# Performance work log

Measured on AMD Instinct MI355X. Metric: run time of the kernel, lower is better.

Reference implementation:

```python
import jax, jax.numpy as jnp
import numpy as np

D_MODEL = 1024
NUM_HEADS = 16
D_K = D_MODEL // NUM_HEADS


def setup_inputs() -> dict:
    key = jax.random.key(0)
    k1, k2, k3 = jax.random.split(key, 3)
    x = jax.random.normal(k1, (2, 2048, D_MODEL), dtype=jnp.float32)
    # torch Linear(d, 3d): weight shape [3d, d], y = x @ W.T
    W_QKV = jax.random.normal(k2, (3 * D_MODEL, D_MODEL), dtype=jnp.float32) * (1.0 / np.sqrt(D_MODEL))
    W_O = jax.random.normal(k3, (D_MODEL, D_MODEL), dtype=jnp.float32) * (1.0 / np.sqrt(D_MODEL))
    return {"x": x, "W_QKV": W_QKV, "W_O": W_O}


def reference(x, W_QKV, W_O):
    B, T, C = x.shape
    qkv = jnp.einsum('btc,fc->btf', x, W_QKV)  # [B,T,3C]
    q, k, v = jnp.split(qkv, 3, axis=-1)
    def heads(t):
        return t.reshape(B, T, NUM_HEADS, D_K).transpose(0, 2, 1, 3)  # [B,H,T,Dk]
    Q, K, V = heads(q), heads(k), heads(v)
    scores = jnp.einsum('bhqd,bhkd->bhqk', Q, K) / jnp.sqrt(jnp.float32(D_K))
    causal = jnp.tril(jnp.ones((T, T), dtype=bool))
    scores = jnp.where(causal, scores, -jnp.inf)
    attn = jax.nn.softmax(scores, axis=-1)
    out = jnp.einsum('bhqk,bhkd->bhqd', attn, V)
    out = out.transpose(0, 2, 1, 3).reshape(B, T, C)
    return jnp.einsum('btc,oc->bto', out, W_O)
```

## Files before the change

### kernel.cpp

```cpp
#include <hip/hip_runtime.h>
#include <hip/hip_bf16.h>
#include <stdint.h>
#include <stddef.h>


typedef __attribute__((ext_vector_type(8)))  __bf16   bf16x8;
typedef __attribute__((ext_vector_type(4)))  float    f32x4;
typedef __attribute__((ext_vector_type(16))) float    f32x16;
typedef __attribute__((ext_vector_type(4)))  uint32_t u32x4;

#define AS1(p) ((__attribute__((address_space(1))) void*)(p))
#define AS3(p) ((__attribute__((address_space(3))) void*)(p))

static constexpr int Tq    = 2048;
static constexpr int Cd    = 1024;
static constexpr int Mrows = 2 * Tq;

#define QSCALE 0.18033688011112042f

__global__ __launch_bounds__(256) void cvt_bf16_kernel(const float* __restrict__ in,
                                                       __bf16* __restrict__ out, int n8)
{
    int idx    = blockIdx.x * blockDim.x + threadIdx.x;
    int stride = gridDim.x * blockDim.x;
    for (int i = idx; i < n8; i += stride) {
        f32x4 a = ((const f32x4*)in)[i * 2 + 0];
        f32x4 b = ((const f32x4*)in)[i * 2 + 1];
        bf16x8 o;
#pragma unroll
        for (int j = 0; j < 4; ++j) { o[j] = (__bf16)a[j]; o[4 + j] = (__bf16)b[j]; }
        ((bf16x8*)out)[i] = o;
    }
}

__global__ __launch_bounds__(256) void transpose_v_kernel(const __bf16* __restrict__ qkv,
                                                          __bf16* __restrict__ vT)
{
    __shared__ __bf16 tile[64][65];
    const int t   = threadIdx.x;
    const int r0  = blockIdx.x * 64;
    const int hd0 = blockIdx.y * 64;

    {
        const int rr = t >> 2, c16 = (t & 3) * 16;
        const __bf16* src = qkv + (size_t)(r0 + rr) * 3072 + 2048 + hd0 + c16;
        bf16x8 a = *(const bf16x8*)(src);
        bf16x8 b = *(const bf16x8*)(src + 8);
#pragma unroll
        for (int j = 0; j < 8; ++j) { tile[rr][c16 + j] = a[j]; tile[rr][c16 + 8 + j] = b[j]; }
    }
    __syncthreads();
    {
        const int hd_loc = t >> 2, rg = (t & 3) * 16;
        bf16x8 a, b;
#pragma unroll
        for (int j = 0; j < 8; ++j) { a[j] = tile[rg + j][hd_loc]; b[j] = tile[rg + 8 + j][hd_loc]; }
        __bf16* dst = vT + (size_t)(hd0 + hd_loc) * Mrows + r0 + rg;
        *(bf16x8*)(dst)     = a;
        *(bf16x8*)(dst + 8) = b;
    }
}

template <bool OUT_BF16>
__global__ __launch_bounds__(256) void gemm_bt_kernel(const __bf16* __restrict__ A,
                                                      const __bf16* __restrict__ Bm,
                                                      float* __restrict__ Cf,
                                                      __bf16* __restrict__ Cb,
                                                      int N, int K, int qcols, float qscale)
{
    __shared__ __align__(16) __bf16 As[128 * 64];
    __shared__ __align__(16) __bf16 Bs[128 * 64];

    const int tid = threadIdx.x;
    const int l   = tid & 63;
    const int w   = tid >> 6;
    const int wr  = w >> 1, wc = w & 1;
    const int lo  = l & 15, hi = l >> 4;
    const int m0  = blockIdx.x * 128;
    const int n0  = blockIdx.y * 128;

    f32x4 acc[4][4] = {};

    for (int kk = 0; kk < K; kk += 64) {
#pragma unroll
        for (int i = 0; i < 4; ++i) {
            int s   = i * 256 + tid;
            int row = s >> 3;
            int gg  = (s & 7) ^ (row & 7);
            const __bf16* srcA = A  + (size_t)(m0 + row) * K + kk + gg * 8;
            const __bf16* srcB = Bm + (size_t)(n0 + row) * K + kk + gg * 8;
            __builtin_amdgcn_global_load_lds(AS1(srcA), AS3((char*)As + s * 16), 16, 0, 0);
            __builtin_amdgcn_global_load_lds(AS1(srcB), AS3((char*)Bs + s * 16), 16, 0, 0);
        }
        __syncthreads();

#pragma unroll
        for (int ks = 0; ks < 2; ++ks) {
            bf16x8 af[4], bfr[4];
#pragma unroll
            for (int m = 0; m < 4; ++m) {
                int row = wr * 64 + m * 16 + lo;
                int gl  = (ks * 4 + hi) ^ (row & 7);
                af[m] = *(const bf16x8*)((const char*)As + row * 128 + gl * 16);
            }
#pragma unroll
            for (int n = 0; n < 4; ++n) {
                int row = wc * 64 + n * 16 + lo;
                int gl  = (ks * 4 + hi) ^ (row & 7);
                bfr[n] = *(const bf16x8*)((const char*)Bs + row * 128 + gl * 16);
            }
#pragma unroll
            for (int m = 0; m < 4; ++m)
#pragma unroll
                for (int n = 0; n < 4; ++n)
                    acc[m][n] = __builtin_amdgcn_mfma_f32_16x16x32_bf16(af[m], bfr[n], acc[m][n], 0, 0, 0);
        }
        __syncthreads();
    }

#pragma unroll
    for (int m = 0; m < 4; ++m)
#pragma unroll
        for (int n = 0; n < 4; ++n)
#pragma unroll
            for (int r = 0; r < 4; ++r) {
                int row = m0 + wr * 64 + m * 16 + hi * 4 + r;
                int col = n0 + wc * 64 + n * 16 + lo;
                float v = acc[m][n][r];
                if (col < qcols) v *= qscale;
                if (OUT_BF16) Cb[(size_t)row * N + col] = (__bf16)v;
                else          Cf[(size_t)row * N + col] = v;
            }
}

__global__ __launch_bounds__(256) void attn_chunk_kernel(const __bf16* __restrict__ qkv,
                                                         const __bf16* __restrict__ vT,
                                                         __bf16* __restrict__ att,
                                                         float* __restrict__ pO,
                                                         float* __restrict__ stats)
{
    constexpr uint8_t QT[24] = { 8, 9,10,11,12,13,14,15,
                                15, 7,14, 6,13, 5,12, 4,
                                11, 3,10, 2, 9, 1, 8, 0};
    constexpr uint8_t CC[24] = { 0, 0, 0, 0, 0, 0, 0, 0,
                                 1,255, 1,255, 1,255, 1,255,
                                 1,255, 1,255, 1,255, 1,255};

    __shared__ __align__(16) __bf16 Ks[2][64 * 64];
    __shared__ __align__(16) __bf16 Vs[2][64 * 64];

    const int tid = threadIdx.x;
    const int l   = tid & 63;
    const int w   = tid >> 6;
    const int lo5 = l & 31, hi5 = l >> 5;

    const int bid = blockIdx.x;
    const int ord = bid >> 5;
    const int bh  = bid & 31;
    const int h   = bh & 15;
    const int b   = bh >> 4;

    const int  qt     = QT[ord];
    const int  cc     = CC[ord];
    const bool direct = (cc == 255);
    const int  ntall  = 2 * qt + 2;
    const int  t0     = direct ? 0 : cc * 16;
    const int  t1     = direct ? ntall : min(cc * 16 + 16, ntall);
    const int  qb0    = qt * 128;

    const __bf16* Kbase = qkv + (size_t)b * Tq * 3072 + 1024 + h * 64;
    const __bf16* Vbase = vT  + (size_t)h * 64 * Mrows + b * Tq;

    bf16x8 onesf;
#pragma unroll
    for (int jj = 0; jj < 8; ++jj) onesf[jj] = (__bf16)1.0f;

    const int qg = qb0 + w * 32 + lo5;

    bf16x8 qf[4];
    {
        const __bf16* Qp = qkv + (size_t)(b * Tq + qg) * 3072 + h * 64 + hi5 * 8;
#pragma unroll
        for (int ds = 0; ds < 4; ++ds) qf[ds] = *(const bf16x8*)(Qp + ds * 16);
    }

    f32x16 o0 = {}, o1 = {}, ls = {};
    float m = -1e30f;

#pragma unroll
    for (int i = 0; i < 2; ++i) {
        int s = i * 256 + tid;
        int row = s >> 3, gg = (s & 7) ^ (row & 7);
        __builtin_amdgcn_global_load_lds(AS1(Kbase + (size_t)(t0 * 64 + row) * 3072 + gg * 8),
                                         AS3((char*)Ks[0] + s * 16), 16, 0, 0);
        __builtin_amdgcn_global_load_lds(AS1(Vbase + (size_t)row * Mrows + t0 * 64 + gg * 8),
                                         AS3((char*)Vs[0] + s * 16), 16, 0, 0);
    }
    __syncthreads();

    int cur = 0;
    for (int t = t0; t < t1; ++t) {
        if (t + 1 < t1) {
            const int kn = (t + 1) * 64;
#pragma unroll
            for (int i = 0; i < 2; ++i) {
                int s = i * 256 + tid;
                int row = s >> 3, gg = (s & 7) ^ (row & 7);
                __builtin_amdgcn_global_load_lds(AS1(Kbase + (size_t)(kn + row) * 3072 + gg * 8),
                                                 AS3((char*)Ks[cur ^ 1] + s * 16), 16, 0, 0);
                __builtin_amdgcn_global_load_lds(AS1(Vbase + (size_t)row * Mrows + kn + gg * 8),
                                                 AS3((char*)Vs[cur ^ 1] + s * 16), 16, 0, 0);
            }
        }

        f32x16 sf0 = {}, sf1 = {};
        __builtin_amdgcn_s_setprio(1);
#pragma unroll
        for (int ds = 0; ds < 4; ++ds) {
            {
                int row = lo5;
                int gl  = (ds * 2 + hi5) ^ (row & 7);
                bf16x8 kf = *(const bf16x8*)((const char*)Ks[cur] + row * 128 + gl * 16);
                sf0 = __builtin_amdgcn_mfma_f32_32x32x16_bf16(kf, qf[ds], sf0, 0, 0, 0);
            }
            {
                int row = 32 + lo5;
                int gl  = (ds * 2 + hi5) ^ (row & 7);
                bf16x8 kf = *(const bf16x8*)((const char*)Ks[cur] + row * 128 + gl * 16);
                sf1 = __builtin_amdgcn_mfma_f32_32x32x16_bf16(kf, qf[ds], sf1, 0, 0, 0);
            }
        }
        __builtin_amdgcn_s_setprio(0);

        if (t * 64 + 63 > qb0 + w * 32) {
#pragma unroll
            for (int r = 0; r < 16; ++r) {
                int kcg = t * 64 + (r & 3) + 8 * (r >> 2) + 4 * hi5;
                if (kcg      > qg) sf0[r] = -1e30f;
                if (kcg + 32 > qg) sf1[r] = -1e30f;
            }
        }

        float t0m = fmaxf(sf0[0],  fmaxf(sf0[1],  sf0[2]));
        float t1m = fmaxf(sf0[3],  fmaxf(sf0[4],  sf0[5]));
        float t2m = fmaxf(sf0[6],  fmaxf(sf0[7],  sf0[8]));
        float t3m = fmaxf(sf0[9],  fmaxf(sf0[10], sf0[11]));
        float t4m = fmaxf(sf0[12], fmaxf(sf0[13], sf0[14]));
        float t5m = fmaxf(sf1[0],  fmaxf(sf1[1],  sf1[2]));
        float t6m = fmaxf(sf1[3],  fmaxf(sf1[4],  sf1[5]));
        float t7m = fmaxf(sf1[6],  fmaxf(sf1[7],  sf1[8]));
        float t8m = fmaxf(sf1[9],  fmaxf(sf1[10], sf1[11]));
        float t9m = fmaxf(sf1[12], fmaxf(sf1[13], sf1[14]));
        float u0 = fmaxf(t0m, fmaxf(t1m, t2m));
        float u1 = fmaxf(t3m, fmaxf(t4m, sf0[15]));
        float u2 = fmaxf(t5m, fmaxf(t6m, t7m));
        float u3 = fmaxf(t8m, fmaxf(t9m, sf1[15]));
        float pmh = fmaxf(fmaxf(u0, u1), fmaxf(u2, u3));
        float pm  = fmaxf(pmh, __shfl_xor(pmh, 32));

        if (__any(pm > m + 8.0f)) {
            float mnew = fmaxf(m, pm);
            float fac  = __builtin_amdgcn_exp2f(m - mnew);
            m = mnew;
#pragma unroll
            for (int r = 0; r < 16; ++r) {
                int qreg = (r & 3) + 8 * (r >> 2) + 4 * hi5;
                float fr = __shfl(fac, qreg);
                o0[r] *= fr;
                o1[r] *= fr;
                ls[r] *= fr;
            }
        }

        __builtin_amdgcn_s_setprio(1);
#pragma unroll
        for (int kb = 0; kb < 2; ++kb) {
            uint32_t W[8];
#pragma unroll
            for (int wd = 0; wd < 8; ++wd) {
                float sa = (kb == 0) ? sf0[2 * wd]     : sf1[2 * wd];
                float sb = (kb == 0) ? sf0[2 * wd + 1] : sf1[2 * wd + 1];
                __bf16 ba = (__bf16)__builtin_amdgcn_exp2f(sa - m);
                __bf16 bb = (__bf16)__builtin_amdgcn_exp2f(sb - m);
                W[wd] = (uint32_t)__builtin_bit_cast(uint16_t, ba)
                      | ((uint32_t)__builtin_bit_cast(uint16_t, bb) << 16);
            }
            uint32_t Za = __shfl_xor(hi5 ? W[0] : W[2], 32);
            uint32_t Zb = __shfl_xor(hi5 ? W[1] : W[3], 32);
            uint32_t Zc = __shfl_xor(hi5 ? W[4] : W[6], 32);
            uint32_t Zd = __shfl_xor(hi5 ? W[5] : W[7], 32);

            {
                u32x4 fw = { hi5 ? Za : W[0], hi5 ? Zb : W[1],
                             hi5 ? W[2] : Za, hi5 ? W[3] : Zb };
                bf16x8 pa = __builtin_bit_cast(bf16x8, fw);
                const int kstep = kb * 2;
                {
                    int row = lo5;
                    int gl  = (kstep * 2 + hi5) ^ (row & 7);
                    bf16x8 vb = *(const bf16x8*)((const char*)Vs[cur] + row * 128 + gl * 16);
                    o0 = __builtin_amdgcn_mfma_f32_32x32x16_bf16(pa, vb, o0, 0, 0, 0);
                }
                {
                    int row = 32 + lo5;
                    int gl  = (kstep * 2 + hi5) ^ (row & 7);
                    bf16x8 vb = *(const bf16x8*)((const char*)Vs[cur] + row * 128 + gl * 16);
                    o1 = __builtin_amdgcn_mfma_f32_32x32x16_bf16(pa, vb, o1, 0, 0, 0);
                }
                ls = __builtin_amdgcn_mfma_f32_32x32x16_bf16(pa, onesf, ls, 0, 0, 0);
            }
            {
                u32x4 fw = { hi5 ? Zc : W[4], hi5 ? Zd : W[5],
                             hi5 ? W[6] : Zc, hi5 ? W[7] : Zd };
                bf16x8 pa = __builtin_bit_cast(bf16x8, fw);
                const int kstep = kb * 2 + 1;
                {
                    int row = lo5;
                    int gl  = (kstep * 2 + hi5) ^ (row & 7);
                    bf16x8 vb = *(const bf16x8*)((const char*)Vs[cur] + row * 128 + gl * 16);
                    o0 = __builtin_amdgcn_mfma_f32_32x32x16_bf16(pa, vb, o0, 0, 0, 0);
                }
                {
                    int row = 32 + lo5;
                    int gl  = (kstep * 2 + hi5) ^ (row & 7);
                    bf16x8 vb = *(const bf16x8*)((const char*)Vs[cur] + row * 128 + gl * 16);
                    o1 = __builtin_amdgcn_mfma_f32_32x32x16_bf16(pa, vb, o1, 0, 0, 0);
                }
                ls = __builtin_amdgcn_mfma_f32_32x32x16_bf16(pa, onesf, ls, 0, 0, 0);
            }
        }
        __builtin_amdgcn_s_setprio(0);

        __syncthreads();
        cur ^= 1;
    }

    if (direct) {
#pragma unroll
        for (int r = 0; r < 16; ++r) {
            float lr   = __builtin_amdgcn_rcpf(ls[r]);
            int   qreg = (r & 3) + 8 * (r >> 2) + 4 * hi5;
            int   rowg = b * Tq + qb0 + w * 32 + qreg;
            att[(size_t)rowg * Cd + h * 64 + lo5]      = (__bf16)(o0[r] * lr);
            att[(size_t)rowg * Cd + h * 64 + 32 + lo5] = (__bf16)(o1[r] * lr);
        }
    } else {
        const int slot = bh * 16 + (qt - 8) * 2 + cc;
        float* po = pO + (size_t)slot * 8192;
#pragma unroll
        for (int r = 0; r < 16; ++r) {
            int   qreg = (r & 3) + 8 * (r >> 2) + 4 * hi5;
            int   row  = w * 32 + qreg;
            po[row * 64 + lo5]      = o0[r];
            po[row * 64 + 32 + lo5] = o1[r];
            float mq = __shfl(m, qreg);
            if (lo5 == 0) {
                stats[(size_t)slot * 256 + row * 2 + 0] = mq;
                stats[(size_t)slot * 256 + row * 2 + 1] = ls[r];
            }
        }
    }
}

__global__ __launch_bounds__(256) void attn_merge_kernel(const float* __restrict__ pO,
                                                         const float* __restrict__ stats,
                                                         __bf16* __restrict__ att)
{
    const int mo  = blockIdx.x;
    const int bh  = mo & 31;
    const int qq  = mo >> 5;
    const int qt  = 8 + qq;
    const int h   = bh & 15;
    const int b   = bh >> 4;

    const int slot0 = bh * 16 + qq * 2;
    const int slot1 = slot0 + 1;

    const int tid = threadIdx.x;
    const int row = tid >> 1;
    const int c0  = (tid & 1) * 32;

    float m0 = stats[(size_t)slot0 * 256 + row * 2 + 0];
    float l0 = stats[(size_t)slot0 * 256 + row * 2 + 1];
    float m1 = stats[(size_t)slot1 * 256 + row * 2 + 0];
    float l1 = stats[(size_t)slot1 * 256 + row * 2 + 1];
    float M  = fmaxf(m0, m1);
    float w0 = exp2f(m0 - M);
    float w1 = exp2f(m1 - M);
    float inv = 1.0f / (w0 * l0 + w1 * l1);

    const float* p0 = pO + (size_t)slot0 * 8192 + row * 64 + c0;
    const float* p1 = pO + (size_t)slot1 * 8192 + row * 64 + c0;

    bf16x8 ov[4];
#pragma unroll
    for (int i = 0; i < 8; ++i) {
        f32x4 a  = ((const f32x4*)p0)[i];
        f32x4 bb = ((const f32x4*)p1)[i];
#pragma unroll
        for (int j = 0; j < 4; ++j)
            ov[i >> 1][(i & 1) * 4 + j] = (__bf16)((w0 * a[j] + w1 * bb[j]) * inv);
    }
    __bf16* dst = att + (size_t)(b * Tq + qt * 128 + row) * Cd + h * 64 + c0;
#pragma unroll
    for (int i = 0; i < 4; ++i) *(bf16x8*)(dst + i * 8) = ov[i];
}

extern "C" void kernel_launch(void* const* d_in, const int* in_sizes, int n_in,
                              void* d_out, int out_size, void* d_ws, size_t ws_size,
                              hipStream_t stream)
{
    (void)in_sizes; (void)n_in; (void)out_size; (void)ws_size;

    const float* x    = (const float*)d_in[0];
    const float* Wqkv = (const float*)d_in[1];
    const float* Wo   = (const float*)d_in[2];
    float*       out  = (float*)d_out;

    char* ws = (char*)d_ws;
    __bf16* xb    = (__bf16*)(ws);
    __bf16* wqkvb = (__bf16*)(ws + (size_t)8  * 1024 * 1024);
    __bf16* wob   = (__bf16*)(ws + (size_t)14 * 1024 * 1024);
    __bf16* qkvb  = (__bf16*)(ws + (size_t)16 * 1024 * 1024);
    __bf16* attb  = (__bf16*)(ws + (size_t)40 * 1024 * 1024);
    __bf16* vTb   = xb;
    float*  stats = (float*)wqkvb;
    float*  pO    = out;

    cvt_bf16_kernel<<<2048, 256, 0, stream>>>(x,    xb,    Mrows * Cd / 8);
    cvt_bf16_kernel<<<1536, 256, 0, stream>>>(Wqkv, wqkvb, 3 * Cd * Cd / 8);
    cvt_bf16_kernel<<<512,  256, 0, stream>>>(Wo,   wob,   Cd * Cd / 8);

    dim3 g1(Mrows / 128, 3 * Cd / 128);
    gemm_bt_kernel<true><<<g1, 256, 0, stream>>>(xb, wqkvb, nullptr, qkvb, 3 * Cd, Cd,
                                                 1024, QSCALE);

    dim3 gt(Mrows / 64, Cd / 64);
    transpose_v_kernel<<<gt, 256, 0, stream>>>(qkvb, vTb);

    attn_chunk_kernel<<<768, 256, 0, stream>>>(qkvb, vTb, attb, pO, stats);
    attn_merge_kernel<<<256, 256, 0, stream>>>(pO, stats, attb);

    dim3 g2(Mrows / 128, Cd / 128);
    gemm_bt_kernel<false><<<g2, 256, 0, stream>>>(attb, wob, out, nullptr, Cd, Cd,
                                                  0, 1.0f);
}
```

Measured before the change: 193.0 us.

## Rebalance causal attention split-KV chunks and store normalized bf16 partials with LSE

```diff
diff --git a/kernel.cpp b/kernel.cpp
--- a/kernel.cpp
+++ b/kernel.cpp
@@ -136,15 +136,21 @@
 __global__ __launch_bounds__(256) void attn_chunk_kernel(const __bf16* __restrict__ qkv,
                                                          const __bf16* __restrict__ vT,
                                                          __bf16* __restrict__ att,
-                                                         float* __restrict__ pO,
+                                                         __bf16* __restrict__ pO,
                                                          float* __restrict__ stats)
 {
-    constexpr uint8_t QT[24] = { 8, 9,10,11,12,13,14,15,
-                                15, 7,14, 6,13, 5,12, 4,
-                                11, 3,10, 2, 9, 1, 8, 0};
-    constexpr uint8_t CC[24] = { 0, 0, 0, 0, 0, 0, 0, 0,
-                                 1,255, 1,255, 1,255, 1,255,
-                                 1,255, 1,255, 1,255, 1,255};
+    constexpr uint8_t QT[36] = {15,15,15,14,14,14,13,13,13,12,12,12,
+                                11,11,11,10, 7, 7, 3,10,10, 9, 9, 6,
+                                 6, 9, 8, 8, 8, 5, 5, 2, 4, 4, 1, 0};
+    constexpr uint8_t T0[36] = { 0,11,22, 0,10,20, 0,10,19, 0, 9,18,
+                                 0, 8,16, 0, 0, 8, 0, 8,15, 0, 7, 0,
+                                 7,14, 0, 6,12, 0, 6, 0, 0, 5, 0, 0};
+    constexpr uint8_t T1[36] = {11,22,32,10,20,30,10,19,28, 9,18,26,
+                                 8,16,24, 8, 8,16, 8,15,22, 7,14, 7,
+                                14,20, 6,12,18, 6,12, 6, 5,10, 4, 2};
+    constexpr uint8_t SL[36] = {29,30,31,26,27,28,23,24,25,20,21,22,
+                                17,18,19,14, 6, 7,255,15,16,11,12, 4,
+                                 5,13, 8, 9,10, 2, 3,255, 0, 1,255,255};
 
     __shared__ __align__(16) __bf16 Ks[2][64 * 64];
     __shared__ __align__(16) __bf16 Vs[2][64 * 64];
@@ -161,11 +167,10 @@
     const int b   = bh >> 4;
 
     const int  qt     = QT[ord];
-    const int  cc     = CC[ord];
-    const bool direct = (cc == 255);
-    const int  ntall  = 2 * qt + 2;
-    const int  t0     = direct ? 0 : cc * 16;
-    const int  t1     = direct ? ntall : min(cc * 16 + 16, ntall);
+    const int  sl     = SL[ord];
+    const bool direct = (sl == 255);
+    const int  t0     = T0[ord];
+    const int  t1     = T1[ord];
     const int  qb0    = qt * 128;
 
     const __bf16* Kbase = qkv + (size_t)b * Tq * 3072 + 1024 + h * 64;
@@ -345,65 +350,72 @@
             att[(size_t)rowg * Cd + h * 64 + 32 + lo5] = (__bf16)(o1[r] * lr);
         }
     } else {
-        const int slot = bh * 16 + (qt - 8) * 2 + cc;
-        float* po = pO + (size_t)slot * 8192;
+        const int slot = bh * 32 + sl;
+        __bf16* po = pO + (size_t)slot * 8192;
 #pragma unroll
         for (int r = 0; r < 16; ++r) {
+            float lr   = __builtin_amdgcn_rcpf(ls[r]);
             int   qreg = (r & 3) + 8 * (r >> 2) + 4 * hi5;
             int   row  = w * 32 + qreg;
-            po[row * 64 + lo5]      = o0[r];
-            po[row * 64 + 32 + lo5] = o1[r];
+            po[row * 64 + lo5]      = (__bf16)(o0[r] * lr);
+            po[row * 64 + 32 + lo5] = (__bf16)(o1[r] * lr);
             float mq = __shfl(m, qreg);
-            if (lo5 == 0) {
-                stats[(size_t)slot * 256 + row * 2 + 0] = mq;
-                stats[(size_t)slot * 256 + row * 2 + 1] = ls[r];
-            }
-        }
-    }
-}
-
-__global__ __launch_bounds__(256) void attn_merge_kernel(const float* __restrict__ pO,
+            if (lo5 == 0)
+                stats[(size_t)slot * 128 + row] = mq + __builtin_amdgcn_logf(ls[r]);
+        }
+    }
+}
+
+__global__ __launch_bounds__(256) void attn_merge_kernel(const __bf16* __restrict__ pO,
                                                          const float* __restrict__ stats,
                                                          __bf16* __restrict__ att)
 {
     const int mo  = blockIdx.x;
     const int bh  = mo & 31;
     const int qq  = mo >> 5;
-    const int qt  = 8 + qq;
+    const int qt  = 4 + qq;
     const int h   = bh & 15;
     const int b   = bh >> 4;
 
-    const int slot0 = bh * 16 + qq * 2;
-    const int slot1 = slot0 + 1;
+    const int ncc   = (qt >= 8) ? 3 : 2;
+    const int slot0 = bh * 32 + ((qt < 8) ? (qt - 4) * 2 : 8 + (qt - 8) * 3);
 
     const int tid = threadIdx.x;
     const int row = tid >> 1;
     const int c0  = (tid & 1) * 32;
 
-    float m0 = stats[(size_t)slot0 * 256 + row * 2 + 0];
-    float l0 = stats[(size_t)slot0 * 256 + row * 2 + 1];
-    float m1 = stats[(size_t)slot1 * 256 + row * 2 + 0];
-    float l1 = stats[(size_t)slot1 * 256 + row * 2 + 1];
-    float M  = fmaxf(m0, m1);
-    float w0 = exp2f(m0 - M);
-    float w1 = exp2f(m1 - M);
-    float inv = 1.0f / (w0 * l0 + w1 * l1);
-
-    const float* p0 = pO + (size_t)slot0 * 8192 + row * 64 + c0;
-    const float* p1 = pO + (size_t)slot1 * 8192 + row * 64 + c0;
-
-    bf16x8 ov[4];
-#pragma unroll
-    for (int i = 0; i < 8; ++i) {
-        f32x4 a  = ((const f32x4*)p0)[i];
-        f32x4 bb = ((const f32x4*)p1)[i];
-#pragma unroll
-        for (int j = 0; j < 4; ++j)
-            ov[i >> 1][(i & 1) * 4 + j] = (__bf16)((w0 * a[j] + w1 * bb[j]) * inv);
-    }
+    float L0 = stats[(size_t)(slot0 + 0) * 128 + row];
+    float L1 = stats[(size_t)(slot0 + 1) * 128 + row];
+    float L2 = (ncc == 3) ? stats[(size_t)(slot0 + 2) * 128 + row] : -1e30f;
+    float M  = fmaxf(L0, fmaxf(L1, L2));
+    float w0 = __builtin_amdgcn_exp2f(L0 - M);
+    float w1 = __builtin_amdgcn_exp2f(L1 - M);
+    float w2 = (ncc == 3) ? __builtin_amdgcn_exp2f(L2 - M) : 0.0f;
+    float inv = 1.0f / (w0 + w1 + w2);
+    w0 *= inv; w1 *= inv; w2 *= inv;
+
+    const __bf16* p0 = pO + (size_t)(slot0 + 0) * 8192 + row * 64 + c0;
+    const __bf16* p1 = pO + (size_t)(slot0 + 1) * 8192 + row * 64 + c0;
+    const __bf16* p2 = pO + (size_t)(slot0 + 2) * 8192 + row * 64 + c0;
+
     __bf16* dst = att + (size_t)(b * Tq + qt * 128 + row) * Cd + h * 64 + c0;
 #pragma unroll
-    for (int i = 0; i < 4; ++i) *(bf16x8*)(dst + i * 8) = ov[i];
+    for (int i = 0; i < 4; ++i) {
+        bf16x8 a = ((const bf16x8*)p0)[i];
+        bf16x8 bb = ((const bf16x8*)p1)[i];
+        bf16x8 ov;
+        if (ncc == 3) {
+            bf16x8 cc = ((const bf16x8*)p2)[i];
+#pragma unroll
+            for (int j = 0; j < 8; ++j)
+                ov[j] = (__bf16)(w0 * (float)a[j] + w1 * (float)bb[j] + w2 * (float)cc[j]);
+        } else {
+#pragma unroll
+            for (int j = 0; j < 8; ++j)
+                ov[j] = (__bf16)(w0 * (float)a[j] + w1 * (float)bb[j]);
+        }
+        ((bf16x8*)dst)[i] = ov;
+    }
 }
 
 extern "C" void kernel_launch(void* const* d_in, const int* in_sizes, int n_in,
@@ -425,7 +437,7 @@
     __bf16* attb  = (__bf16*)(ws + (size_t)40 * 1024 * 1024);
     __bf16* vTb   = xb;
     float*  stats = (float*)wqkvb;
-    float*  pO    = out;
+    __bf16* pO    = (__bf16*)out;
 
     cvt_bf16_kernel<<<2048, 256, 0, stream>>>(x,    xb,    Mrows * Cd / 8);
     cvt_bf16_kernel<<<1536, 256, 0, stream>>>(Wqkv, wqkvb, 3 * Cd * Cd / 8);
@@ -438,8 +450,8 @@
     dim3 gt(Mrows / 64, Cd / 64);
     transpose_v_kernel<<<gt, 256, 0, stream>>>(qkvb, vTb);
 
-    attn_chunk_kernel<<<768, 256, 0, stream>>>(qkvb, vTb, attb, pO, stats);
-    attn_merge_kernel<<<256, 256, 0, stream>>>(pO, stats, attb);
+    attn_chunk_kernel<<<1152, 256, 0, stream>>>(qkvb, vTb, attb, pO, stats);
+    attn_merge_kernel<<<384, 256, 0, stream>>>(pO, stats, attb);
 
     dim3 g2(Mrows / 128, Cd / 128);
     gemm_bt_kernel<false><<<g2, 256, 0, stream>>>(attb, wob, out, nullptr, Cd, Cd,
```

Result: no change. 193.8 us (+0.4%).

## Double-buffer GEMM LDS tiles to overlap global loads with MFMA

Applied to the files above, without the earlier changes.

```diff
diff --git a/kernel.cpp b/kernel.cpp
--- a/kernel.cpp
+++ b/kernel.cpp
@@ -68,8 +68,8 @@
                                                       __bf16* __restrict__ Cb,
                                                       int N, int K, int qcols, float qscale)
 {
-    __shared__ __align__(16) __bf16 As[128 * 64];
-    __shared__ __align__(16) __bf16 Bs[128 * 64];
+    __shared__ __align__(16) __bf16 As[2][128 * 64];
+    __shared__ __align__(16) __bf16 Bs[2][128 * 64];
 
     const int tid = threadIdx.x;
     const int l   = tid & 63;
@@ -81,19 +81,34 @@
 
     f32x4 acc[4][4] = {};
 
+#pragma unroll
+    for (int i = 0; i < 4; ++i) {
+        int s   = i * 256 + tid;
+        int row = s >> 3;
+        int gg  = (s & 7) ^ (row & 7);
+        __builtin_amdgcn_global_load_lds(AS1(A  + (size_t)(m0 + row) * K + gg * 8),
+                                         AS3((char*)As[0] + s * 16), 16, 0, 0);
+        __builtin_amdgcn_global_load_lds(AS1(Bm + (size_t)(n0 + row) * K + gg * 8),
+                                         AS3((char*)Bs[0] + s * 16), 16, 0, 0);
+    }
+    __syncthreads();
+
+    int cur = 0;
     for (int kk = 0; kk < K; kk += 64) {
-#pragma unroll
-        for (int i = 0; i < 4; ++i) {
-            int s   = i * 256 + tid;
-            int row = s >> 3;
-            int gg  = (s & 7) ^ (row & 7);
-            const __bf16* srcA = A  + (size_t)(m0 + row) * K + kk + gg * 8;
-            const __bf16* srcB = Bm + (size_t)(n0 + row) * K + kk + gg * 8;
-            __builtin_amdgcn_global_load_lds(AS1(srcA), AS3((char*)As + s * 16), 16, 0, 0);
-            __builtin_amdgcn_global_load_lds(AS1(srcB), AS3((char*)Bs + s * 16), 16, 0, 0);
-        }
-        __syncthreads();
-
+        if (kk + 64 < K) {
+#pragma unroll
+            for (int i = 0; i < 4; ++i) {
+                int s   = i * 256 + tid;
+                int row = s >> 3;
+                int gg  = (s & 7) ^ (row & 7);
+                __builtin_amdgcn_global_load_lds(AS1(A  + (size_t)(m0 + row) * K + kk + 64 + gg * 8),
+                                                 AS3((char*)As[cur ^ 1] + s * 16), 16, 0, 0);
+                __builtin_amdgcn_global_load_lds(AS1(Bm + (size_t)(n0 + row) * K + kk + 64 + gg * 8),
+                                                 AS3((char*)Bs[cur ^ 1] + s * 16), 16, 0, 0);
+            }
+        }
+
+        __builtin_amdgcn_s_setprio(1);
 #pragma unroll
         for (int ks = 0; ks < 2; ++ks) {
             bf16x8 af[4], bfr[4];
@@ -101,13 +116,13 @@
             for (int m = 0; m < 4; ++m) {
                 int row = wr * 64 + m * 16 + lo;
                 int gl  = (ks * 4 + hi) ^ (row & 7);
-                af[m] = *(const bf16x8*)((const char*)As + row * 128 + gl * 16);
+                af[m] = *(const bf16x8*)((const char*)As[cur] + row * 128 + gl * 16);
             }
 #pragma unroll
             for (int n = 0; n < 4; ++n) {
                 int row = wc * 64 + n * 16 + lo;
                 int gl  = (ks * 4 + hi) ^ (row & 7);
-                bfr[n] = *(const bf16x8*)((const char*)Bs + row * 128 + gl * 16);
+                bfr[n] = *(const bf16x8*)((const char*)Bs[cur] + row * 128 + gl * 16);
             }
 #pragma unroll
             for (int m = 0; m < 4; ++m)
@@ -115,7 +130,10 @@
                 for (int n = 0; n < 4; ++n)
                     acc[m][n] = __builtin_amdgcn_mfma_f32_16x16x32_bf16(af[m], bfr[n], acc[m][n], 0, 0, 0);
         }
+        __builtin_amdgcn_s_setprio(0);
+
         __syncthreads();
+        cur ^= 1;
     }
 
 #pragma unroll
@@ -385,8 +403,8 @@
     float m1 = stats[(size_t)slot1 * 256 + row * 2 + 0];
     float l1 = stats[(size_t)slot1 * 256 + row * 2 + 1];
     float M  = fmaxf(m0, m1);
-    float w0 = exp2f(m0 - M);
-    float w1 = exp2f(m1 - M);
+    float w0 = __builtin_amdgcn_exp2f(m0 - M);
+    float w1 = __builtin_amdgcn_exp2f(m1 - M);
     float inv = 1.0f / (w0 * l0 + w1 * l1);
 
     const float* p0 = pO + (size_t)slot0 * 8192 + row * 64 + c0;
```

Measured after the change: 198.0 us. +2.6%, slower.
